# Kernel optimization log

Measured on AMD Instinct MI355X. Metric: run time of the kernel, lower is better.

Reference implementation:

```python
import jax, jax.numpy as jnp
import numpy as np

B, S, V, D = 64, 256, 50000, 300
NW, CL, CV, CD = 8192, 16, 500, 30
H, T, CH = 128, 17, 30


def setup_inputs() -> dict:
    key = jax.random.key(0)
    ks = jax.random.split(key, 32)
    f32 = jnp.float32
    def rn(k, shape, scale=0.1):
        return jax.random.normal(k, shape, dtype=f32) * scale
    inp = {}
    inp["char_emb"] = rn(ks[0], (CV, CD)).at[0].set(0.0)  # padding_idx=0
    inp["conv_w"] = rn(ks[1], (CH, CD, 3))  # OIH
    inp["conv_b"] = rn(ks[2], (CH,))
    inp["word_emb"] = rn(ks[3], (V, D))
    in0, in1 = D + CH, 2 * H
    inp["w_ih_l0"] = rn(ks[4], (2, 3 * H, in0))  # [dir, 3H, in]
    inp["w_hh_l0"] = rn(ks[5], (2, 3 * H, H))
    inp["b_ih_l0"] = rn(ks[6], (2, 3 * H))
    inp["b_hh_l0"] = rn(ks[7], (2, 3 * H))
    inp["w_ih_l1"] = rn(ks[8], (2, 3 * H, in1))
    inp["w_hh_l1"] = rn(ks[9], (2, 3 * H, H))
    inp["b_ih_l1"] = rn(ks[10], (2, 3 * H))
    inp["b_hh_l1"] = rn(ks[11], (2, 3 * H))
    inp["mlp_w1"] = rn(ks[12], (2 * H, H))
    inp["mlp_b1"] = rn(ks[13], (H,))
    inp["mlp_w2"] = rn(ks[14], (H, T))
    inp["mlp_b2"] = rn(ks[15], (T,))
    inp["crf_start"] = rn(ks[16], (T,))
    inp["crf_end"] = rn(ks[17], (T,))
    inp["crf_trans"] = rn(ks[18], (T, T))
    inp["batched_char_words"] = jax.random.randint(ks[19], (NW, CL), 0, CV)
    inp["batched_char_words_len"] = jax.random.randint(ks[20], (NW,), 1, CL + 1)
    inp["batched_char_word_index"] = jax.random.randint(ks[21], (B, S), 0, NW + 1)
    inp["batched_tokens"] = jax.random.randint(ks[22], (B, S), 0, V)
    inp["batched_tokens_len"] = jax.random.randint(ks[23], (B,), S // 2, S + 1)
    inp["target"] = jax.random.randint(ks[24], (B, S), 0, T)
    return inp


def _gru_dir(x, mask, w_ih, w_hh, b_ih, b_hh, reverse):
    # x: [B,S,I], mask: [B,S] bool. Masked (padded) steps carry hidden state
    # through unchanged, matching pack_padded_sequence semantics.
    xg = jnp.einsum('bsi,gi->sbg', x, w_ih) + b_ih  # [S,B,3H]
    m = mask.T  # [S,B]
    h0 = jnp.zeros((x.shape[0], w_hh.shape[1]), x.dtype)

    def step(h, inp):
        xt, mt = inp
        hg = h @ w_hh.T + b_hh
        xr, xz, xn = jnp.split(xt, 3, axis=-1)
        hr, hz, hn = jnp.split(hg, 3, axis=-1)
        r = jax.nn.sigmoid(xr + hr)
        z = jax.nn.sigmoid(xz + hz)
        n = jnp.tanh(xn + r * hn)
        hnew = (1.0 - z) * n + z * h
        h = jnp.where(mt[:, None], hnew, h)
        return h, h

    _, hs = jax.lax.scan(step, h0, (xg, m), reverse=reverse)
    return hs.transpose(1, 0, 2)  # [B,S,H]


def _bigru_layer(x, mask, w_ih, w_hh, b_ih, b_hh):
    fwd = _gru_dir(x, mask, w_ih[0], w_hh[0], b_ih[0], b_hh[0], False)
    bwd = _gru_dir(x, mask, w_ih[1], w_hh[1], b_ih[1], b_hh[1], True)
    return jnp.concatenate([fwd, bwd], axis=-1)


def _forward(char_emb, conv_w, conv_b, word_emb,
             w_ih_l0, w_hh_l0, b_ih_l0, b_hh_l0,
             w_ih_l1, w_hh_l1, b_ih_l1, b_hh_l1,
             mlp_w1, mlp_b1, mlp_w2, mlp_b2,
             crf_start, crf_end, crf_trans,
             batched_char_words, batched_char_word_index,
             batched_tokens, batched_tokens_len, target):
    # --- char CNN token encoder: conv1d(k=3, SAME) + relu + max-over-time ---
    ct = char_emb[batched_char_words]  # [NW,CL,CD]
    c = jax.lax.conv_general_dilated(ct.transpose(0, 2, 1), conv_w, (1,), 'SAME',
                                     dimension_numbers=('NCH', 'OIH', 'NCH'))
    c = jax.nn.relu(c + conv_b[None, :, None])
    tok_enc = jnp.max(c, axis=-1)  # [NW,CH]
    tok_enc = jnp.concatenate([jnp.zeros((1, tok_enc.shape[1]), tok_enc.dtype), tok_enc], axis=0)
    tok_idx = tok_enc[batched_char_word_index]  # [B,S,CH] (index 0 -> zeros)

    texts = jnp.concatenate([word_emb[batched_tokens], tok_idx], axis=-1)  # [B,S,D+CH]
    seq = batched_tokens.shape[1]
    mask = jnp.arange(seq)[None, :] < batched_tokens_len[:, None]  # [B,S]

    # --- 2-layer BiGRU ---
    h = _bigru_layer(texts, mask, w_ih_l0, w_hh_l0, b_ih_l0, b_hh_l0)
    h = _bigru_layer(h, mask, w_ih_l1, w_hh_l1, b_ih_l1, b_hh_l1)

    # --- MLP head -> emissions [B,S,17] ---
    h = jax.nn.relu(h @ mlp_w1 + mlp_b1)
    emissions = h @ mlp_w2 + mlp_b2

    # --- CRF negative log-likelihood, reduction='token_mean' ---
    maskf = mask.astype(emissions.dtype)
    emit_sc = jnp.take_along_axis(emissions, target[..., None], axis=-1)[..., 0]  # [B,S]
    trans_sc = crf_trans[target[:, :-1], target[:, 1:]]  # [B,S-1]
    score = crf_start[target[:, 0]] + emit_sc[:, 0]
    score = score + jnp.sum((trans_sc + emit_sc[:, 1:]) * maskf[:, 1:], axis=1)
    last_tags = jnp.take_along_axis(target, (batched_tokens_len - 1)[:, None], axis=1)[:, 0]
    score = score + crf_end[last_tags]

    alpha0 = crf_start[None, :] + emissions[:, 0]  # [B,T]
    em_rest = emissions[:, 1:].transpose(1, 0, 2)  # [S-1,B,T]
    m_rest = mask[:, 1:].T  # [S-1,B]

    def crf_step(alpha, inp):
        emit, mt = inp
        new = jax.nn.logsumexp(alpha[:, :, None] + crf_trans[None], axis=1) + emit
        return jnp.where(mt[:, None], new, alpha), None

    alpha, _ = jax.lax.scan(crf_step, alpha0, (em_rest, m_rest))
    log_z = jax.nn.logsumexp(alpha + crf_end[None, :], axis=1)
    llh = score - log_z
    return -(jnp.sum(llh) / jnp.sum(maskf))


def reference(char_emb, conv_w, conv_b, word_emb,
              w_ih_l0, w_hh_l0, b_ih_l0, b_hh_l0,
              w_ih_l1, w_hh_l1, b_ih_l1, b_hh_l1,
              mlp_w1, mlp_b1, mlp_w2, mlp_b2,
              crf_start, crf_end, crf_trans,
              batched_char_words, batched_char_words_len,
              batched_char_word_index, batched_tokens, batched_tokens_len, target):
    return _forward(char_emb, conv_w, conv_b, word_emb,
                    w_ih_l0, w_hh_l0, b_ih_l0, b_hh_l0,
                    w_ih_l1, w_hh_l1, b_ih_l1, b_hh_l1,
                    mlp_w1, mlp_b1, mlp_w2, mlp_b2,
                    crf_start, crf_end, crf_trans,
                    batched_char_words, batched_char_word_index,
                    batched_tokens, batched_tokens_len, target)
```

## Files before the change

kernel.cpp:

```cpp
#include <hip/hip_runtime.h>
#include <cstddef>

#define BATCH 64
#define SEQ   256
#define VOCAB 50000
#define DIM   300
#define NW    8192
#define CLEN  16
#define CDIM  30
#define CHC   30
#define HID   128
#define NT    17
#define IN0   (DIM + CHC)
#define IN0P  336
#define IN1   (2 * HID)
#define NPOS  (BATCH * SEQ)

constexpr size_t SZ_XG    = 2ull * BATCH * SEQ * 384;
constexpr size_t SZ_TEXTS = (size_t)NPOS * IN0P;
constexpr size_t SZ_H1    = (size_t)NPOS * 256;
constexpr size_t SZ_TOK   = 245792;
constexpr size_t SZ_EMIS  = (size_t)NPOS * NT;
constexpr size_t SZ_WPAD  = 768ull * IN0P;
constexpr size_t OFF_XG    = 0;
constexpr size_t OFF_TEXTS = OFF_XG + SZ_XG;
constexpr size_t OFF_H1    = OFF_TEXTS + SZ_TEXTS;
constexpr size_t OFF_TOK   = OFF_H1 + SZ_H1;
constexpr size_t OFF_EMIS  = OFF_TOK + SZ_TOK;
constexpr size_t OFF_WPAD  = OFF_EMIS + SZ_EMIS;
constexpr size_t OFF_LLH   = OFF_WPAD + SZ_WPAD;

__device__ __forceinline__ float sigm(float x) {
    return 1.f / (1.f + __expf(-x));
}
__device__ __forceinline__ float tanh_fast(float x) {
    x = fminf(fmaxf(x, -15.f), 15.f);
    float e = __expf(-2.f * x);
    return (1.f - e) / (1.f + e);
}
__device__ __forceinline__ float quad_sum(float x) {
    int y = __builtin_amdgcn_update_dpp(0, __float_as_int(x), 0xB1, 0xF, 0xF, false);
    x += __int_as_float(y);
    y = __builtin_amdgcn_update_dpp(0, __float_as_int(x), 0x4E, 0xF, 0xF, false);
    x += __int_as_float(y);
    return x;
}

__global__ __launch_bounds__(256) void char_conv_k(
    const float* __restrict__ char_emb,
    const float* __restrict__ conv_w,
    const float* __restrict__ conv_b,
    const int*   __restrict__ words,
    float* __restrict__ tok_enc)
{
    __shared__ __align__(16) float cs[8][CLEN][CDIM];
    __shared__ float wsm[CHC * CDIM * 3];
    __shared__ float bs[CHC];
    int n0 = blockIdx.x * 8;
    int tid = threadIdx.x;
    for (int e = tid; e < CHC * CDIM * 3; e += 256) wsm[e] = conv_w[e];
    if (tid < CHC) bs[tid] = conv_b[tid];
    for (int e = tid; e < 8 * CLEN * CDIM; e += 256) {
        int wi = e / (CLEN * CDIM);
        int rem = e - wi * (CLEN * CDIM);
        int l = rem / CDIM;
        int i = rem - l * CDIM;
        int ci = words[(n0 + wi) * CLEN + l];
        cs[wi][l][i] = char_emb[ci * CDIM + i];
    }
    __syncthreads();
    int wi = tid >> 5;
    int o = tid & 31;
    if (o < CHC) {
        float best = -1e30f;
        for (int l = 0; l < CLEN; l++) {
            float s = 0.f;
            #pragma unroll
            for (int k = 0; k < 3; k++) {
                int ll = l + k - 1;
                if (ll >= 0 && ll < CLEN) {
                    #pragma unroll
                    for (int i = 0; i < CDIM; i++)
                        s += cs[wi][ll][i] * wsm[(o * CDIM + i) * 3 + k];
                }
            }
            best = fmaxf(best, s);
        }
        tok_enc[(size_t)(n0 + wi + 1) * CDIM + o] = fmaxf(best + bs[o], 0.f);
    }
}

__global__ __launch_bounds__(128) void build_texts_k(
    const float* __restrict__ word_emb,
    const float* __restrict__ tok_enc,
    const int*   __restrict__ tokens,
    const int*   __restrict__ widx,
    float* __restrict__ texts)
{
    int p = blockIdx.x;
    int tok = tokens[p];
    int ci = widx[p];
    float* o = texts + (size_t)p * IN0P;
    const float* wr = word_emb + (size_t)tok * DIM;
    const float* tr = tok_enc + (size_t)ci * CDIM;
    for (int c = threadIdx.x; c < IN0P; c += 128)
        o[c] = (c < DIM) ? wr[c] : (c < IN0 ? tr[c - DIM] : 0.f);
}

__global__ __launch_bounds__(64) void pad_w_k(
    const float* __restrict__ w, float* __restrict__ wp)
{
    int r = blockIdx.x;
    for (int c = threadIdx.x; c < IN0P; c += 64)
        wp[(size_t)r * IN0P + c] = (c < IN0) ? w[(size_t)r * IN0 + c] : 0.f;
}

#define GBM 128
#define GBN 128
#define GBK 16
__global__ __launch_bounds__(256) void gemm_xg_k(
    const float* __restrict__ A,
    const float* __restrict__ W,
    const float* __restrict__ bias,
    float* __restrict__ out,
    int K)
{
    __shared__ __align__(16) float As[GBK][GBM];
    __shared__ __align__(16) float Ws[GBK][GBN];
    int tid = threadIdx.x;
    int m0 = blockIdx.x * GBM;
    int n0 = blockIdx.y * GBN;
    int lrow = tid >> 1;
    int lk = (tid & 1) * 8;
    int ty = tid >> 4;
    int tx = tid & 15;

    float acc[8][8];
    #pragma unroll
    for (int i = 0; i < 8; i++)
        #pragma unroll
        for (int j = 0; j < 8; j++) acc[i][j] = 0.f;

    for (int k0 = 0; k0 < K; k0 += GBK) {
        const float4* ap = (const float4*)(A + (size_t)(m0 + lrow) * K + k0 + lk);
        const float4* wp = (const float4*)(W + (size_t)(n0 + lrow) * K + k0 + lk);
        float4 va0 = ap[0], va1 = ap[1];
        float4 vw0 = wp[0], vw1 = wp[1];
        As[lk + 0][lrow] = va0.x; As[lk + 1][lrow] = va0.y;
        As[lk + 2][lrow] = va0.z; As[lk + 3][lrow] = va0.w;
        As[lk + 4][lrow] = va1.x; As[lk + 5][lrow] = va1.y;
        As[lk + 6][lrow] = va1.z; As[lk + 7][lrow] = va1.w;
        Ws[lk + 0][lrow] = vw0.x; Ws[lk + 1][lrow] = vw0.y;
        Ws[lk + 2][lrow] = vw0.z; Ws[lk + 3][lrow] = vw0.w;
        Ws[lk + 4][lrow] = vw1.x; Ws[lk + 5][lrow] = vw1.y;
        Ws[lk + 6][lrow] = vw1.z; Ws[lk + 7][lrow] = vw1.w;
        __syncthreads();
        #pragma unroll
        for (int k = 0; k < GBK; k++) {
            float4 a0 = *(const float4*)&As[k][ty * 8];
            float4 a1 = *(const float4*)&As[k][ty * 8 + 4];
            float4 b0 = *(const float4*)&Ws[k][tx * 8];
            float4 b1 = *(const float4*)&Ws[k][tx * 8 + 4];
            float av[8] = {a0.x, a0.y, a0.z, a0.w, a1.x, a1.y, a1.z, a1.w};
            float bv[8] = {b0.x, b0.y, b0.z, b0.w, b1.x, b1.y, b1.z, b1.w};
            #pragma unroll
            for (int i = 0; i < 8; i++)
                #pragma unroll
                for (int j = 0; j < 8; j++)
                    acc[i][j] += av[i] * bv[j];
        }
        __syncthreads();
    }
    int nb = n0 + tx * 8;
    int d = nb / 384;
    int g0 = nb - d * 384;
    float bvv[8];
    #pragma unroll
    for (int j = 0; j < 8; j++) bvv[j] = bias[nb + j];
    int mbase = m0 + ty * 8;
    #pragma unroll
    for (int i = 0; i < 8; i++) {
        int m = mbase + i;
        int b = m >> 8;
        int t = m & 255;
        float* op = out + (((size_t)(d * BATCH + b) * SEQ + t) * 384 + g0);
        #pragma unroll
        for (int j = 0; j < 8; j++) op[j] = acc[i][j] + bvv[j];
    }
}

__global__ __launch_bounds__(512, 2) void gru_rec_k(
    const float* __restrict__ xg,
    const float* __restrict__ w_hh,
    const float* __restrict__ b_hh,
    const int*   __restrict__ lens,
    float* __restrict__ out)
{
    int d = blockIdx.x & 1;
    int b = blockIdx.x >> 1;
    int i = threadIdx.x;
    int e = i >> 2;
    int c = i & 3;
    __shared__ __align__(16) float hS[2][HID];

    int rR = e, rZ = HID + e, rN = 2 * HID + e;
    const float* wbR = w_hh + ((size_t)d * 384 + rR) * HID + 32 * c;
    const float* wbZ = w_hh + ((size_t)d * 384 + rZ) * HID + 32 * c;
    const float* wbN = w_hh + ((size_t)d * 384 + rN) * HID + 32 * c;
    float4 wR[8], wZ[8], wN[8];
    #pragma unroll
    for (int q = 0; q < 8; q++) {
        int m = (q + c) & 7;
        wR[q] = *(const float4*)(wbR + 4 * m);
        wZ[q] = *(const float4*)(wbZ + 4 * m);
        wN[q] = *(const float4*)(wbN + 4 * m);
    }
    float bhR = b_hh[d * 384 + rR];
    float bhZ = b_hh[d * 384 + rZ];
    float bhN = b_hh[d * 384 + rN];
    int len = lens[b];

    if (i < HID) { hS[0][i] = 0.f; }
    float hold = 0.f;
    __syncthreads();

    const float* xgb = xg + ((size_t)(d * BATCH + b)) * SEQ * 384;
    float* outb = out + (size_t)b * SEQ * 256 + d * HID;

    int t0 = d ? (SEQ - 1) : 0;
    float xvR = xgb[(size_t)t0 * 384 + rR];
    float xvZ = xgb[(size_t)t0 * 384 + rZ];
    float xvN = xgb[(size_t)t0 * 384 + rN];
    int tPrev = 0;

    for (int s = 0; s < SEQ; s++) {
        int t = d ? (SEQ - 1 - s) : s;
        if (s && c == 0) outb[(size_t)tPrev * 256 + e] = hold;
        int sn = (s + 1 < SEQ) ? (s + 1) : s;
        int tn = d ? (SEQ - 1 - sn) : sn;
        float nxvR = xgb[(size_t)tn * 384 + rR];
        float nxvZ = xgb[(size_t)tn * 384 + rZ];
        float nxvN = xgb[(size_t)tn * 384 + rN];

        const float4* hb = (const float4*)hS[s & 1] + 8 * c;
        float sR = 0.f, sZ = 0.f, sN = 0.f;
        #pragma unroll
        for (int q = 0; q < 8; q++) {
            int m = (q + c) & 7;
            float4 hv = hb[m];
            sR += wR[q].x * hv.x + wR[q].y * hv.y + wR[q].z * hv.z + wR[q].w * hv.w;
            sZ += wZ[q].x * hv.x + wZ[q].y * hv.y + wZ[q].z * hv.z + wZ[q].w * hv.w;
            sN += wN[q].x * hv.x + wN[q].y * hv.y + wN[q].z * hv.z + wN[q].w * hv.w;
        }
        sR = quad_sum(sR);
        sZ = quad_sum(sZ);
        sN = quad_sum(sN);

        float r = sigm(xvR + sR + bhR);
        float z = sigm(xvZ + sZ + bhZ);
        float n = tanh_fast(xvN + r * (sN + bhN));
        float hnew = (1.f - z) * n + z * hold;
        hold = (t < len) ? hnew : hold;
        if (c == 0) hS[(s & 1) ^ 1][e] = hold;
        tPrev = t;
        xvR = nxvR; xvZ = nxvZ; xvN = nxvN;
        __syncthreads();
    }
    if (c == 0) outb[(size_t)tPrev * 256 + e] = hold;
}

__global__ __launch_bounds__(128) void mlp_emis_k(
    const float* __restrict__ h1,
    const float* __restrict__ w1,
    const float* __restrict__ b1,
    const float* __restrict__ w2,
    const float* __restrict__ b2,
    float* __restrict__ emis)
{
    __shared__ __align__(16) float hrow[8 * 256];
    __shared__ float hid[8][HID];
    int p0 = blockIdx.x * 8;
    int tid = threadIdx.x;
    for (int e = tid; e < 8 * 256; e += 128)
        hrow[e] = h1[(size_t)p0 * 256 + e];
    __syncthreads();
    float acc[8];
    float bb = b1[tid];
    #pragma unroll
    for (int i = 0; i < 8; i++) acc[i] = bb;
    for (int k = 0; k < 256; k++) {
        float wv = w1[k * HID + tid];
        #pragma unroll
        for (int i = 0; i < 8; i++) acc[i] += hrow[i * 256 + k] * wv;
    }
    #pragma unroll
    for (int i = 0; i < 8; i++) hid[i][tid] = fmaxf(acc[i], 0.f);
    __syncthreads();
    for (int idx = tid; idx < 8 * NT; idx += 128) {
        int pos = idx / NT;
        int tg = idx - pos * NT;
        float a = b2[tg];
        for (int k = 0; k < HID; k++) a += hid[pos][k] * w2[k * NT + tg];
        emis[(size_t)(p0 + pos) * NT + tg] = a;
    }
}

__global__ __launch_bounds__(64) void crf_k(
    const float* __restrict__ emis,
    const float* __restrict__ start,
    const float* __restrict__ endv,
    const float* __restrict__ trans,
    const int*   __restrict__ target,
    const int*   __restrict__ lens,
    float* __restrict__ llh)
{
    int b = blockIdx.x;
    int tid = threadIdx.x;
    __shared__ float tr[NT * NT];
    __shared__ float aSh[NT];
    __shared__ float scoreSh;
    for (int e = tid; e < NT * NT; e += 64) tr[e] = trans[e];
    __syncthreads();
    int len = lens[b];
    const int* tgt = target + b * SEQ;
    const float* eb = emis + (size_t)b * SEQ * NT;

    float part = 0.f;
    for (int t = 1 + tid; t < SEQ; t += 64) {
        if (t < len) {
            int tp = tgt[t - 1], tc = tgt[t];
            part += tr[tp * NT + tc] + eb[(size_t)t * NT + tc];
        }
    }
    #pragma unroll
    for (int off = 32; off > 0; off >>= 1)
        part += __shfl_down(part, off, 64);
    if (tid == 0) {
        int t0 = tgt[0];
        scoreSh = part + start[t0] + eb[t0] + endv[tgt[len - 1]];
    }

    float a = (tid < NT) ? (start[tid] + eb[tid]) : 0.f;
    for (int t = 1; t < SEQ; t++) {
        if (tid < NT) aSh[tid] = a;
        __syncthreads();
        if (t < len && tid < NT) {
            float m = -1e30f;
            #pragma unroll
            for (int i = 0; i < NT; i++)
                m = fmaxf(m, aSh[i] + tr[i * NT + tid]);
            float ssum = 0.f;
            #pragma unroll
            for (int i = 0; i < NT; i++)
                ssum += __expf(aSh[i] + tr[i * NT + tid] - m);
            a = m + __logf(ssum) + eb[(size_t)t * NT + tid];
        }
        __syncthreads();
    }
    float v = (tid < NT) ? (a + endv[tid]) : -1e30f;
    float m = v;
    #pragma unroll
    for (int off = 32; off > 0; off >>= 1)
        m = fmaxf(m, __shfl_down(m, off, 64));
    m = __shfl(m, 0, 64);
    float e = (tid < NT) ? __expf(v - m) : 0.f;
    #pragma unroll
    for (int off = 32; off > 0; off >>= 1)
        e += __shfl_down(e, off, 64);
    if (tid == 0) {
        float logz = m + __logf(e);
        llh[b] = scoreSh - logz;
    }
}

__global__ __launch_bounds__(64) void finalize_k(
    const float* __restrict__ llh,
    const int*   __restrict__ lens,
    float* __restrict__ out)
{
    int tid = threadIdx.x;
    float s = llh[tid];
    float lf = (float)lens[tid];
    #pragma unroll
    for (int off = 32; off > 0; off >>= 1) {
        s += __shfl_down(s, off, 64);
        lf += __shfl_down(lf, off, 64);
    }
    if (tid == 0) out[0] = -(s / lf);
}

extern "C" void kernel_launch(void* const* d_in, const int* in_sizes, int n_in,
                              void* d_out, int out_size, void* d_ws, size_t ws_size,
                              hipStream_t stream) {
    const float* char_emb = (const float*)d_in[0];
    const float* conv_w   = (const float*)d_in[1];
    const float* conv_b   = (const float*)d_in[2];
    const float* word_emb = (const float*)d_in[3];
    const float* w_ih_l0  = (const float*)d_in[4];
    const float* w_hh_l0  = (const float*)d_in[5];
    const float* b_ih_l0  = (const float*)d_in[6];
    const float* b_hh_l0  = (const float*)d_in[7];
    const float* w_ih_l1  = (const float*)d_in[8];
    const float* w_hh_l1  = (const float*)d_in[9];
    const float* b_ih_l1  = (const float*)d_in[10];
    const float* b_hh_l1  = (const float*)d_in[11];
    const float* mlp_w1   = (const float*)d_in[12];
    const float* mlp_b1   = (const float*)d_in[13];
    const float* mlp_w2   = (const float*)d_in[14];
    const float* mlp_b2   = (const float*)d_in[15];
    const float* crf_start= (const float*)d_in[16];
    const float* crf_end  = (const float*)d_in[17];
    const float* crf_trans= (const float*)d_in[18];
    const int* bcw   = (const int*)d_in[19];
    const int* bcwi  = (const int*)d_in[21];
    const int* btok  = (const int*)d_in[22];
    const int* blen  = (const int*)d_in[23];
    const int* target= (const int*)d_in[24];

    float* ws    = (float*)d_ws;
    float* xg    = ws + OFF_XG;
    float* texts = ws + OFF_TEXTS;
    float* h0    = texts;
    float* h1    = ws + OFF_H1;
    float* tok   = ws + OFF_TOK;
    float* emis  = ws + OFF_EMIS;
    float* wpad  = ws + OFF_WPAD;
    float* llh   = ws + OFF_LLH;

    hipMemsetAsync(tok, 0, CDIM * sizeof(float), stream);
    pad_w_k<<<768, 64, 0, stream>>>(w_ih_l0, wpad);
    char_conv_k<<<NW / 8, 256, 0, stream>>>(char_emb, conv_w, conv_b, bcw, tok);
    build_texts_k<<<NPOS, 128, 0, stream>>>(word_emb, tok, btok, bcwi, texts);
    gemm_xg_k<<<dim3(NPOS / GBM, 768 / GBN), 256, 0, stream>>>(texts, wpad, b_ih_l0, xg, IN0P);
    gru_rec_k<<<2 * BATCH, 512, 0, stream>>>(xg, w_hh_l0, b_hh_l0, blen, h0);
    gemm_xg_k<<<dim3(NPOS / GBM, 768 / GBN), 256, 0, stream>>>(h0, w_ih_l1, b_ih_l1, xg, IN1);
    gru_rec_k<<<2 * BATCH, 512, 0, stream>>>(xg, w_hh_l1, b_hh_l1, blen, h1);
    mlp_emis_k<<<NPOS / 8, 128, 0, stream>>>(h1, mlp_w1, mlp_b1, mlp_w2, mlp_b2, emis);
    crf_k<<<BATCH, 64, 0, stream>>>(emis, crf_start, crf_end, crf_trans, target, blen, llh);
    finalize_k<<<1, 64, 0, stream>>>(llh, blen, (float*)d_out);
}
```

Measured before the change: 879.5 us.

## Pad GEMM weight tile in LDS and use packed FMA in GRU recurrence

The input-projection GEMM now stores its weight tile in shared memory with padded, swizzled columns, meant to cut LDS bank conflicts on the float4 reads. The GRU recurrence keeps its weight registers as two-wide float vectors and accumulates with elementwise FMA so the compiler can emit packed v_pk_fma_f32 instructions, halving the FMA instruction count on the serial critical path. The packed accumulation changes summation order slightly and may change register allocation.

```diff
diff --git a/kernel.cpp b/kernel.cpp
--- a/kernel.cpp
+++ b/kernel.cpp
@@ -29,6 +29,8 @@
 constexpr size_t OFF_EMIS  = OFF_TOK + SZ_TOK;
 constexpr size_t OFF_WPAD  = OFF_EMIS + SZ_EMIS;
 constexpr size_t OFF_LLH   = OFF_WPAD + SZ_WPAD;
+
+typedef float float2v __attribute__((ext_vector_type(2)));
 
 __device__ __forceinline__ float sigm(float x) {
     return 1.f / (1.f + __expf(-x));
@@ -118,6 +120,7 @@
 #define GBM 128
 #define GBN 128
 #define GBK 16
+#define GBNP 132
 __global__ __launch_bounds__(256) void gemm_xg_k(
     const float* __restrict__ A,
     const float* __restrict__ W,
@@ -126,7 +129,7 @@
     int K)
 {
     __shared__ __align__(16) float As[GBK][GBM];
-    __shared__ __align__(16) float Ws[GBK][GBN];
+    __shared__ __align__(16) float Ws[GBK][GBNP];
     int tid = threadIdx.x;
     int m0 = blockIdx.x * GBM;
     int n0 = blockIdx.y * GBN;
@@ -134,6 +137,8 @@
     int lk = (tid & 1) * 8;
     int ty = tid >> 4;
     int tx = tid & 15;
+    int wcol = lrow + 4 * ((lrow >> 5) & 1);
+    int bbase = tx * 8 + 4 * ((tx >> 2) & 1);
 
     float acc[8][8];
     #pragma unroll
@@ -150,17 +155,17 @@
         As[lk + 2][lrow] = va0.z; As[lk + 3][lrow] = va0.w;
         As[lk + 4][lrow] = va1.x; As[lk + 5][lrow] = va1.y;
         As[lk + 6][lrow] = va1.z; As[lk + 7][lrow] = va1.w;
-        Ws[lk + 0][lrow] = vw0.x; Ws[lk + 1][lrow] = vw0.y;
-        Ws[lk + 2][lrow] = vw0.z; Ws[lk + 3][lrow] = vw0.w;
-        Ws[lk + 4][lrow] = vw1.x; Ws[lk + 5][lrow] = vw1.y;
-        Ws[lk + 6][lrow] = vw1.z; Ws[lk + 7][lrow] = vw1.w;
+        Ws[lk + 0][wcol] = vw0.x; Ws[lk + 1][wcol] = vw0.y;
+        Ws[lk + 2][wcol] = vw0.z; Ws[lk + 3][wcol] = vw0.w;
+        Ws[lk + 4][wcol] = vw1.x; Ws[lk + 5][wcol] = vw1.y;
+        Ws[lk + 6][wcol] = vw1.z; Ws[lk + 7][wcol] = vw1.w;
         __syncthreads();
         #pragma unroll
         for (int k = 0; k < GBK; k++) {
             float4 a0 = *(const float4*)&As[k][ty * 8];
             float4 a1 = *(const float4*)&As[k][ty * 8 + 4];
-            float4 b0 = *(const float4*)&Ws[k][tx * 8];
-            float4 b1 = *(const float4*)&Ws[k][tx * 8 + 4];
+            float4 b0 = *(const float4*)&Ws[k][bbase];
+            float4 b1 = *(const float4*)&Ws[k][bbase + 4];
             float av[8] = {a0.x, a0.y, a0.z, a0.w, a1.x, a1.y, a1.z, a1.w};
             float bv[8] = {b0.x, b0.y, b0.z, b0.w, b1.x, b1.y, b1.z, b1.w};
             #pragma unroll
@@ -207,20 +212,23 @@
     const float* wbR = w_hh + ((size_t)d * 384 + rR) * HID + 32 * c;
     const float* wbZ = w_hh + ((size_t)d * 384 + rZ) * HID + 32 * c;
     const float* wbN = w_hh + ((size_t)d * 384 + rN) * HID + 32 * c;
-    float4 wR[8], wZ[8], wN[8];
+    float2v wR[16], wZ[16], wN[16];
     #pragma unroll
     for (int q = 0; q < 8; q++) {
         int m = (q + c) & 7;
-        wR[q] = *(const float4*)(wbR + 4 * m);
-        wZ[q] = *(const float4*)(wbZ + 4 * m);
-        wN[q] = *(const float4*)(wbN + 4 * m);
+        float4 tR = *(const float4*)(wbR + 4 * m);
+        float4 tZ = *(const float4*)(wbZ + 4 * m);
+        float4 tN = *(const float4*)(wbN + 4 * m);
+        wR[2 * q].x = tR.x; wR[2 * q].y = tR.y; wR[2 * q + 1].x = tR.z; wR[2 * q + 1].y = tR.w;
+        wZ[2 * q].x = tZ.x; wZ[2 * q].y = tZ.y; wZ[2 * q + 1].x = tZ.z; wZ[2 * q + 1].y = tZ.w;
+        wN[2 * q].x = tN.x; wN[2 * q].y = tN.y; wN[2 * q + 1].x = tN.z; wN[2 * q + 1].y = tN.w;
     }
     float bhR = b_hh[d * 384 + rR];
     float bhZ = b_hh[d * 384 + rZ];
     float bhN = b_hh[d * 384 + rN];
     int len = lens[b];
 
-    if (i < HID) { hS[0][i] = 0.f; }
+    if (i < HID) hS[0][i] = 0.f;
     float hold = 0.f;
     __syncthreads();
 
@@ -243,18 +251,23 @@
         float nxvN = xgb[(size_t)tn * 384 + rN];
 
         const float4* hb = (const float4*)hS[s & 1] + 8 * c;
-        float sR = 0.f, sZ = 0.f, sN = 0.f;
+        float2v aR = {0.f, 0.f}, aZ = {0.f, 0.f}, aN = {0.f, 0.f};
         #pragma unroll
         for (int q = 0; q < 8; q++) {
             int m = (q + c) & 7;
             float4 hv = hb[m];
-            sR += wR[q].x * hv.x + wR[q].y * hv.y + wR[q].z * hv.z + wR[q].w * hv.w;
-            sZ += wZ[q].x * hv.x + wZ[q].y * hv.y + wZ[q].z * hv.z + wZ[q].w * hv.w;
-            sN += wN[q].x * hv.x + wN[q].y * hv.y + wN[q].z * hv.z + wN[q].w * hv.w;
+            float2v hlo; hlo.x = hv.x; hlo.y = hv.y;
+            float2v hhi; hhi.x = hv.z; hhi.y = hv.w;
+            aR = __builtin_elementwise_fma(wR[2 * q], hlo, aR);
+            aR = __builtin_elementwise_fma(wR[2 * q + 1], hhi, aR);
+            aZ = __builtin_elementwise_fma(wZ[2 * q], hlo, aZ);
+            aZ = __builtin_elementwise_fma(wZ[2 * q + 1], hhi, aZ);
+            aN = __builtin_elementwise_fma(wN[2 * q], hlo, aN);
+            aN = __builtin_elementwise_fma(wN[2 * q + 1], hhi, aN);
         }
-        sR = quad_sum(sR);
-        sZ = quad_sum(sZ);
-        sN = quad_sum(sN);
+        float sR = quad_sum(aR.x + aR.y);
+        float sZ = quad_sum(aZ.x + aZ.y);
+        float sN = quad_sum(aN.x + aN.y);
 
         float r = sigm(xvR + sR + bhR);
         float z = sigm(xvZ + sZ + bhZ);
```

New measurement: 894.2 us. No clear change (+1.7%).
